# Optimization experiments

Hardware: AMD Instinct MI355X
Metric: run time of the kernel (lower is better)

The kernel has to match this reference:

```python
import jax, jax.numpy as jnp
import numpy as np

B, H, L, DK, DV = 2, 16, 2048, 64, 64


def setup_inputs() -> dict:
    key = jax.random.key(0)
    kq, kk, kv, km = jax.random.split(key, 4)
    return {
        "Q": jax.random.normal(kq, (B, H, L, DK), dtype=jnp.float32),
        "K": jax.random.normal(kk, (B, H, L, DK), dtype=jnp.float32),
        "V": jax.random.normal(kv, (B, H, L, DV), dtype=jnp.float32),
        "attn_mask": jax.random.uniform(km, (L, L), dtype=jnp.float32),
        "d_k": DK,
    }


def reference(Q, K, V, attn_mask, d_k):
    # scores: [B, H, L, L]
    scale = 1.0 / np.sqrt(d_k).astype(np.float32)
    scores = jnp.einsum("bhqd,bhkd->bhqk", Q, K) * scale
    attn = jax.nn.softmax(scores, axis=-1)
    # MSE-style loss vs a 2-D target mask broadcast over (B, H)
    diff = attn - attn_mask[None, None, :, :]
    loss = jnp.sum(diff * diff)
    context = jnp.einsum("bhqk,bhkd->bhqd", attn, V)
    return (context, loss)
```

## Files before the change

kernel.cpp:

```cpp
#include <hip/hip_runtime.h>

#define NHEAD 32
#define LSEQ  2048
#define DIM   64
#define QBLK  64
#define KBLK  64
#define NTILE (LSEQ / KBLK)

typedef float  f32x4  __attribute__((ext_vector_type(4)));
typedef __bf16 bf16x8 __attribute__((ext_vector_type(8)));
typedef unsigned short u16;

__device__ __forceinline__ u16 f2bf(float f) {
    return __builtin_bit_cast(u16, (__bf16)f);
}
__device__ __forceinline__ void st4bf(u16* p, float4 v) {
    union { u16 h[4]; uint2 q; } pk;
    pk.h[0] = f2bf(v.x); pk.h[1] = f2bf(v.y);
    pk.h[2] = f2bf(v.z); pk.h[3] = f2bf(v.w);
    *(uint2*)p = pk.q;
}
__device__ __forceinline__ bf16x8 comb64(const u16* a, const u16* b) {
    union { uint2 q[2]; bf16x8 v; } u;
    u.q[0] = *(const uint2*)a;
    u.q[1] = *(const uint2*)b;
    return u.v;
}

#define QSCALE 0.18033688011112042f
#define RESCALE_THR 8.0f

__launch_bounds__(256, 4)
__global__ void attn_fused_kernel(const float* __restrict__ Q,
                                  const float* __restrict__ K,
                                  const float* __restrict__ V,
                                  const float* __restrict__ Msk,
                                  float* __restrict__ out,
                                  float* __restrict__ loss)
{
    __shared__ __align__(16) u16 lds_k[64][72];
    __shared__ __align__(16) u16 lds_v[64][68];

    const int t  = threadIdx.x;
    const int wg   = ((int)blockIdx.x & 7) * 128 + ((int)blockIdx.x >> 3);
    const int head = wg >> 5;
    const int qb   = wg & 31;
    const int qbase = qb * QBLK;
    const int w  = t >> 6;
    const int l  = t & 63;
    const int lr = l & 15;
    const int lq = l >> 4;

    const size_t hoff = (size_t)head * LSEQ * DIM;
    const int qg = qbase + 16 * w + lr;

    bf16x8 qf[2];
#pragma unroll
    for (int s = 0; s < 2; ++s) {
        const float* src = Q + hoff + (size_t)qg * DIM + 32 * s + 8 * lq;
        float4 a = *(const float4*)(src);
        float4 b = *(const float4*)(src + 4);
        union { u16 h[8]; bf16x8 v; } u;
        u.h[0] = f2bf(a.x * QSCALE); u.h[1] = f2bf(a.y * QSCALE);
        u.h[2] = f2bf(a.z * QSCALE); u.h[3] = f2bf(a.w * QSCALE);
        u.h[4] = f2bf(b.x * QSCALE); u.h[5] = f2bf(b.y * QSCALE);
        u.h[6] = f2bf(b.z * QSCALE); u.h[7] = f2bf(b.w * QSCALE);
        qf[s] = u.v;
    }

    f32x4 acc[4];
#pragma unroll
    for (int dt = 0; dt < 4; ++dt) acc[dt] = (f32x4){0.f, 0.f, 0.f, 0.f};
    float mrun = -1e30f, lrun = 0.f, la2 = 0.f, lam = 0.f;

    for (int kb = 0; kb < NTILE; ++kb) {
        const int kbase = kb * KBLK;
        __syncthreads();

        f32x4 mreg[4];
        {
            const float* mp_ = Msk + (size_t)qg * LSEQ + kbase + 4 * lq;
#pragma unroll
            for (int m = 0; m < 4; ++m)
                mreg[m] = *(const f32x4*)(mp_ + 16 * m);
        }

        {
            const float* Kg = K + hoff + (size_t)kbase * DIM;
            const float* Vg = V + hoff + (size_t)kbase * DIM;
#pragma unroll
            for (int i = 0; i < 4; ++i) {
                const int id = t + 256 * i;
                const int r = id >> 4, c = (id & 15) * 4;
                float4 kv = *(const float4*)(Kg + r * DIM + c);
                float4 vv = *(const float4*)(Vg + r * DIM + c);
                st4bf(&lds_k[r][c], kv);
                lds_v[c + 0][r] = f2bf(vv.x);
                lds_v[c + 1][r] = f2bf(vv.y);
                lds_v[c + 2][r] = f2bf(vv.z);
                lds_v[c + 3][r] = f2bf(vv.w);
            }
        }
        __syncthreads();

        f32x4 S[4];
#pragma unroll
        for (int m = 0; m < 4; ++m) {
            bf16x8 kf0 = *(const bf16x8*)&lds_k[16 * m + lr][8 * lq];
            bf16x8 kf1 = *(const bf16x8*)&lds_k[16 * m + lr][32 + 8 * lq];
            f32x4 z = (f32x4){0.f, 0.f, 0.f, 0.f};
            z = __builtin_amdgcn_mfma_f32_16x16x32_bf16(kf0, qf[0], z, 0, 0, 0);
            z = __builtin_amdgcn_mfma_f32_16x16x32_bf16(kf1, qf[1], z, 0, 0, 0);
            S[m] = z;
        }

        float tm = fmaxf(fmaxf(fmaxf(S[0][0], S[0][1]), fmaxf(S[0][2], S[0][3])),
                         fmaxf(fmaxf(S[1][0], S[1][1]), fmaxf(S[1][2], S[1][3])));
        tm = fmaxf(tm, fmaxf(fmaxf(fmaxf(S[2][0], S[2][1]), fmaxf(S[2][2], S[2][3])),
                             fmaxf(fmaxf(S[3][0], S[3][1]), fmaxf(S[3][2], S[3][3]))));
        tm = fmaxf(tm, __shfl_xor(tm, 16));
        tm = fmaxf(tm, __shfl_xor(tm, 32));
        if (!__all(tm - mrun <= RESCALE_THR)) {
            const float mn = fmaxf(mrun, tm);
            const float al = __builtin_amdgcn_exp2f(mrun - mn);
            mrun = mn;
            lrun *= al; la2 *= al * al; lam *= al;
#pragma unroll
            for (int dt = 0; dt < 4; ++dt) acc[dt] *= al;
        }

        float psum = 0.f, pp2 = 0.f, ppm = 0.f;
        u16 pb[16];
#pragma unroll
        for (int m = 0; m < 4; ++m) {
#pragma unroll
            for (int r = 0; r < 4; ++r) {
                float p = __builtin_amdgcn_exp2f(S[m][r] - mrun);
                psum += p;
                pp2  += p * p;
                ppm  += p * mreg[m][r];
                pb[4 * m + r] = f2bf(p);
            }
        }
        lrun += psum; la2 += pp2; lam += ppm;

        bf16x8 pf[2];
#pragma unroll
        for (int mp = 0; mp < 2; ++mp) {
            union { u16 h[8]; bf16x8 v; } u;
#pragma unroll
            for (int j = 0; j < 4; ++j) { u.h[j] = pb[8 * mp + j]; u.h[4 + j] = pb[8 * mp + 4 + j]; }
            pf[mp] = u.v;
        }
#pragma unroll
        for (int dt = 0; dt < 4; ++dt) {
#pragma unroll
            for (int mp = 0; mp < 2; ++mp) {
                bf16x8 vf = comb64(&lds_v[16 * dt + lr][32 * mp + 4 * lq],
                                   &lds_v[16 * dt + lr][32 * mp + 16 + 4 * lq]);
                acc[dt] = __builtin_amdgcn_mfma_f32_16x16x32_bf16(vf, pf[mp], acc[dt], 0, 0, 0);
            }
        }
    }

#pragma unroll
    for (int off = 16; off <= 32; off <<= 1) {
        lrun += __shfl_xor(lrun, off);
        la2  += __shfl_xor(la2,  off);
        lam  += __shfl_xor(lam,  off);
    }

    const float inv = 1.0f / lrun;

#pragma unroll
    for (int dt = 0; dt < 4; ++dt) {
        float4 o;
        o.x = acc[dt][0] * inv; o.y = acc[dt][1] * inv;
        o.z = acc[dt][2] * inv; o.w = acc[dt][3] * inv;
        *(float4*)(out + hoff + (size_t)qg * DIM + 16 * dt + 4 * lq) = o;
    }

    float part = la2 * inv * inv - 2.0f * lam * inv;
    part = (l < 16) ? part : 0.f;
#pragma unroll
    for (int off = 1; off <= 8; off <<= 1) part += __shfl_xor(part, off);
    if (l == 0) atomicAdd(loss, part);
}

__global__ void masksq_kernel(const float* __restrict__ Msk, float* __restrict__ loss)
{
    __shared__ float red[4];
    float s = 0.f;
    const size_t n4 = (size_t)LSEQ * LSEQ / 4;
    for (size_t i = (size_t)blockIdx.x * blockDim.x + threadIdx.x; i < n4;
         i += (size_t)gridDim.x * blockDim.x) {
        float4 v = ((const float4*)Msk)[i];
        s += v.x * v.x + v.y * v.y + v.z * v.z + v.w * v.w;
    }
#pragma unroll
    for (int off = 1; off <= 32; off <<= 1) s += __shfl_xor(s, off);
    if ((threadIdx.x & 63) == 0) red[threadIdx.x >> 6] = s;
    __syncthreads();
    if (threadIdx.x == 0) {
        float tot = red[0] + red[1] + red[2] + red[3];
        atomicAdd(loss, 32.0f * tot);
    }
}

extern "C" void kernel_launch(void* const* d_in, const int* in_sizes, int n_in,
                              void* d_out, int out_size, void* d_ws, size_t ws_size,
                              hipStream_t stream)
{
    const float* Q   = (const float*)d_in[0];
    const float* K   = (const float*)d_in[1];
    const float* V   = (const float*)d_in[2];
    const float* Msk = (const float*)d_in[3];
    float* out  = (float*)d_out;
    float* loss = out + (size_t)NHEAD * LSEQ * DIM;

    hipMemsetAsync(loss, 0, sizeof(float), stream);
    masksq_kernel<<<256, 256, 0, stream>>>(Msk, loss);
    attn_fused_kernel<<<NHEAD * (LSEQ / QBLK), 256, 0, stream>>>(Q, K, V, Msk, out, loss);
}
```

Baseline: 147.6 us.

## Prepack K/V to swizzled bf16 tiles and double-buffer via direct global-to-LDS loads

Adds a prepack kernel that converts K and V to bf16 once per call, using an XOR-swizzled tile layout with V already transposed, and writes them to the workspace. The attention kernel then streams each tile into double-buffered LDS with global_load_lds, prefetching the next tile while computing the current one. It also raises wave priority around the MFMA blocks. This removes the 32x redundant fp32 K/V conversion per query block and halves K/V read traffic, at the cost of an extra launch, workspace use, and twice the LDS per block. Without enough workspace it falls back to the old kernel.

Measured after the change: 147.1 us. No clear change (-0.4%).

```diff
diff --git a/kernel.cpp b/kernel.cpp
--- a/kernel.cpp
+++ b/kernel.cpp
@@ -27,19 +27,77 @@
     return u.v;
 }
 
+__device__ __forceinline__ void gl_lds16(const u16* g, u16* l) {
+    __builtin_amdgcn_global_load_lds(
+        (const __attribute__((address_space(1))) void*)g,
+        (__attribute__((address_space(3))) void*)l, 16, 0, 0);
+}
+
+#define TILE_SYNC() asm volatile("s_waitcnt vmcnt(0)\n\ts_barrier" ::: "memory")
+
 #define QSCALE 0.18033688011112042f
 #define RESCALE_THR 8.0f
 
+__global__ void prepack_kernel(const float* __restrict__ K,
+                               const float* __restrict__ V,
+                               u16* __restrict__ wsK, u16* __restrict__ wsV)
+{
+    __shared__ float sv[64][65];
+    const int b = blockIdx.x;
+    const int head = b >> 5, kb = b & 31;
+    const int t = threadIdx.x;
+    const size_t hoff = (size_t)head * LSEQ * DIM;
+    const float* Kg = K + hoff + (size_t)(kb * KBLK) * DIM;
+    const float* Vg = V + hoff + (size_t)(kb * KBLK) * DIM;
+    u16* outK = wsK + (size_t)b * 4096;
+    u16* outV = wsV + (size_t)b * 4096;
+
+#pragma unroll
+    for (int i = 0; i < 16; ++i) {
+        const int e = t + 256 * i;
+        sv[e >> 6][e & 63] = Vg[e];
+    }
+#pragma unroll
+    for (int i = 0; i < 2; ++i) {
+        const int c = t + 256 * i;
+        const int r = c >> 3, q = c & 7;
+        const int d0 = 8 * (q ^ (r & 7));
+        float4 a  = *(const float4*)(Kg + r * DIM + d0);
+        float4 bb = *(const float4*)(Kg + r * DIM + d0 + 4);
+        union { u16 h[8]; uint4 u; } pk;
+        pk.h[0]=f2bf(a.x);  pk.h[1]=f2bf(a.y);  pk.h[2]=f2bf(a.z);  pk.h[3]=f2bf(a.w);
+        pk.h[4]=f2bf(bb.x); pk.h[5]=f2bf(bb.y); pk.h[6]=f2bf(bb.z); pk.h[7]=f2bf(bb.w);
+        *(uint4*)(outK + c * 8) = pk.u;
+    }
+    __syncthreads();
+#pragma unroll
+    for (int i = 0; i < 2; ++i) {
+        const int c = t + 256 * i;
+        const int d = c >> 3, q = c & 7;
+        const int cl = q ^ (d & 7);
+        const int mp = cl >> 2, lq = cl & 3;
+        union { u16 h[8]; uint4 u; } pk;
+#pragma unroll
+        for (int s = 0; s < 2; ++s) {
+            const int k0 = 4 * (8 * mp + 4 * s + lq);
+#pragma unroll
+            for (int j = 0; j < 4; ++j)
+                pk.h[4 * s + j] = f2bf(sv[k0 + j][d]);
+        }
+        *(uint4*)(outV + c * 8) = pk.u;
+    }
+}
+
 __launch_bounds__(256, 4)
 __global__ void attn_fused_kernel(const float* __restrict__ Q,
-                                  const float* __restrict__ K,
-                                  const float* __restrict__ V,
+                                  const u16* __restrict__ wsK,
+                                  const u16* __restrict__ wsV,
                                   const float* __restrict__ Msk,
                                   float* __restrict__ out,
                                   float* __restrict__ loss)
 {
-    __shared__ __align__(16) u16 lds_k[64][72];
-    __shared__ __align__(16) u16 lds_v[64][68];
+    __shared__ __align__(16) u16 lds_k[2][4096];
+    __shared__ __align__(16) u16 lds_v[2][4096];
 
     const int t  = threadIdx.x;
     const int wg   = ((int)blockIdx.x & 7) * 128 + ((int)blockIdx.x >> 3);
@@ -50,6 +108,7 @@
     const int l  = t & 63;
     const int lr = l & 15;
     const int lq = l >> 4;
+    const int x7 = lr & 7;
 
     const size_t hoff = (size_t)head * LSEQ * DIM;
     const int qg = qbase + 16 * w + lr;
@@ -73,10 +132,170 @@
     for (int dt = 0; dt < 4; ++dt) acc[dt] = (f32x4){0.f, 0.f, 0.f, 0.f};
     float mrun = -1e30f, lrun = 0.f, la2 = 0.f, lam = 0.f;
 
+    const u16* srcK = wsK + (size_t)(head * NTILE) * 4096 + t * 8;
+    const u16* srcV = wsV + (size_t)(head * NTILE) * 4096 + t * 8;
+
+    auto stage = [&](int buf, int kb) {
+        const u16* gk = srcK + (size_t)kb * 4096;
+        const u16* gv = srcV + (size_t)kb * 4096;
+        gl_lds16(gk,        &lds_k[buf][t * 8]);
+        gl_lds16(gk + 2048, &lds_k[buf][t * 8 + 2048]);
+        gl_lds16(gv,        &lds_v[buf][t * 8]);
+        gl_lds16(gv + 2048, &lds_v[buf][t * 8 + 2048]);
+    };
+
+    stage(0, 0);
+    int cur = 0;
+
+    for (int kb = 0; kb < NTILE; ++kb) {
+        TILE_SYNC();
+
+        f32x4 mreg[4];
+        {
+            const float* mp_ = Msk + (size_t)qg * LSEQ + kb * KBLK + 4 * lq;
+#pragma unroll
+            for (int m = 0; m < 4; ++m)
+                mreg[m] = *(const f32x4*)(mp_ + 16 * m);
+        }
+
+        if (kb + 1 < NTILE) stage(cur ^ 1, kb + 1);
+
+        f32x4 S[4];
+        __builtin_amdgcn_s_setprio(1);
+#pragma unroll
+        for (int m = 0; m < 4; ++m) {
+            const u16* kro = &lds_k[cur][(16 * m + lr) * 64];
+            bf16x8 kf0 = *(const bf16x8*)(kro + ((lq ^ x7) << 3));
+            bf16x8 kf1 = *(const bf16x8*)(kro + (((lq + 4) ^ x7) << 3));
+            f32x4 z = (f32x4){0.f, 0.f, 0.f, 0.f};
+            z = __builtin_amdgcn_mfma_f32_16x16x32_bf16(kf0, qf[0], z, 0, 0, 0);
+            z = __builtin_amdgcn_mfma_f32_16x16x32_bf16(kf1, qf[1], z, 0, 0, 0);
+            S[m] = z;
+        }
+        __builtin_amdgcn_s_setprio(0);
+
+        float tm = fmaxf(fmaxf(fmaxf(S[0][0], S[0][1]), fmaxf(S[0][2], S[0][3])),
+                         fmaxf(fmaxf(S[1][0], S[1][1]), fmaxf(S[1][2], S[1][3])));
+        tm = fmaxf(tm, fmaxf(fmaxf(fmaxf(S[2][0], S[2][1]), fmaxf(S[2][2], S[2][3])),
+                             fmaxf(fmaxf(S[3][0], S[3][1]), fmaxf(S[3][2], S[3][3]))));
+        tm = fmaxf(tm, __shfl_xor(tm, 16));
+        tm = fmaxf(tm, __shfl_xor(tm, 32));
+        if (!__all(tm - mrun <= RESCALE_THR)) {
+            const float mn = fmaxf(mrun, tm);
+            const float al = __builtin_amdgcn_exp2f(mrun - mn);
+            mrun = mn;
+            lrun *= al; la2 *= al * al; lam *= al;
+#pragma unroll
+            for (int dt = 0; dt < 4; ++dt) acc[dt] *= al;
+        }
+
+        float psum = 0.f, pp2 = 0.f, ppm = 0.f;
+        u16 pb[16];
+#pragma unroll
+        for (int m = 0; m < 4; ++m) {
+#pragma unroll
+            for (int r = 0; r < 4; ++r) {
+                float p = __builtin_amdgcn_exp2f(S[m][r] - mrun);
+                psum += p;
+                pp2  += p * p;
+                ppm  += p * mreg[m][r];
+                pb[4 * m + r] = f2bf(p);
+            }
+        }
+        lrun += psum; la2 += pp2; lam += ppm;
+
+        bf16x8 pf[2];
+#pragma unroll
+        for (int mp = 0; mp < 2; ++mp) {
+            union { u16 h[8]; bf16x8 v; } u;
+#pragma unroll
+            for (int j = 0; j < 4; ++j) { u.h[j] = pb[8 * mp + j]; u.h[4 + j] = pb[8 * mp + 4 + j]; }
+            pf[mp] = u.v;
+        }
+        __builtin_amdgcn_s_setprio(1);
+#pragma unroll
+        for (int dt = 0; dt < 4; ++dt) {
+            const u16* vro = &lds_v[cur][(16 * dt + lr) * 64];
+#pragma unroll
+            for (int mp = 0; mp < 2; ++mp) {
+                bf16x8 vf = *(const bf16x8*)(vro + (((4 * mp + lq) ^ x7) << 3));
+                acc[dt] = __builtin_amdgcn_mfma_f32_16x16x32_bf16(vf, pf[mp], acc[dt], 0, 0, 0);
+            }
+        }
+        __builtin_amdgcn_s_setprio(0);
+        cur ^= 1;
+    }
+
+#pragma unroll
+    for (int off = 16; off <= 32; off <<= 1) {
+        lrun += __shfl_xor(lrun, off);
+        la2  += __shfl_xor(la2,  off);
+        lam  += __shfl_xor(lam,  off);
+    }
+
+    const float inv = 1.0f / lrun;
+
+#pragma unroll
+    for (int dt = 0; dt < 4; ++dt) {
+        float4 o;
+        o.x = acc[dt][0] * inv; o.y = acc[dt][1] * inv;
+        o.z = acc[dt][2] * inv; o.w = acc[dt][3] * inv;
+        *(float4*)(out + hoff + (size_t)qg * DIM + 16 * dt + 4 * lq) = o;
+    }
+
+    float part = la2 * inv * inv - 2.0f * lam * inv;
+    part = (l < 16) ? part : 0.f;
+#pragma unroll
+    for (int off = 1; off <= 8; off <<= 1) part += __shfl_xor(part, off);
+    if (l == 0) atomicAdd(loss, part);
+}
+
+__launch_bounds__(256, 4)
+__global__ void attn_fallback_kernel(const float* __restrict__ Q,
+                                     const float* __restrict__ K,
+                                     const float* __restrict__ V,
+                                     const float* __restrict__ Msk,
+                                     float* __restrict__ out,
+                                     float* __restrict__ loss)
+{
+    __shared__ __align__(16) u16 lds_k[64][72];
+    __shared__ __align__(16) u16 lds_v[64][68];
+
+    const int t  = threadIdx.x;
+    const int wg   = ((int)blockIdx.x & 7) * 128 + ((int)blockIdx.x >> 3);
+    const int head = wg >> 5;
+    const int qb   = wg & 31;
+    const int qbase = qb * QBLK;
+    const int w  = t >> 6;
+    const int l  = t & 63;
+    const int lr = l & 15;
+    const int lq = l >> 4;
+
+    const size_t hoff = (size_t)head * LSEQ * DIM;
+    const int qg = qbase + 16 * w + lr;
+
+    bf16x8 qf[2];
+#pragma unroll
+    for (int s = 0; s < 2; ++s) {
+        const float* src = Q + hoff + (size_t)qg * DIM + 32 * s + 8 * lq;
+        float4 a = *(const float4*)(src);
+        float4 b = *(const float4*)(src + 4);
+        union { u16 h[8]; bf16x8 v; } u;
+        u.h[0] = f2bf(a.x * QSCALE); u.h[1] = f2bf(a.y * QSCALE);
+        u.h[2] = f2bf(a.z * QSCALE); u.h[3] = f2bf(a.w * QSCALE);
+        u.h[4] = f2bf(b.x * QSCALE); u.h[5] = f2bf(b.y * QSCALE);
+        u.h[6] = f2bf(b.z * QSCALE); u.h[7] = f2bf(b.w * QSCALE);
+        qf[s] = u.v;
+    }
+
+    f32x4 acc[4];
+#pragma unroll
+    for (int dt = 0; dt < 4; ++dt) acc[dt] = (f32x4){0.f, 0.f, 0.f, 0.f};
+    float mrun = -1e30f, lrun = 0.f, la2 = 0.f, lam = 0.f;
+
     for (int kb = 0; kb < NTILE; ++kb) {
         const int kbase = kb * KBLK;
         __syncthreads();
-
         f32x4 mreg[4];
         {
             const float* mp_ = Msk + (size_t)qg * LSEQ + kbase + 4 * lq;
@@ -84,7 +303,6 @@
             for (int m = 0; m < 4; ++m)
                 mreg[m] = *(const f32x4*)(mp_ + 16 * m);
         }
-
         {
             const float* Kg = K + hoff + (size_t)kbase * DIM;
             const float* Vg = V + hoff + (size_t)kbase * DIM;
@@ -169,9 +387,7 @@
         la2  += __shfl_xor(la2,  off);
         lam  += __shfl_xor(lam,  off);
     }
-
     const float inv = 1.0f / lrun;
-
 #pragma unroll
     for (int dt = 0; dt < 4; ++dt) {
         float4 o;
@@ -179,7 +395,6 @@
         o.z = acc[dt][2] * inv; o.w = acc[dt][3] * inv;
         *(float4*)(out + hoff + (size_t)qg * DIM + 16 * dt + 4 * lq) = o;
     }
-
     float part = la2 * inv * inv - 2.0f * lam * inv;
     part = (l < 16) ? part : 0.f;
 #pragma unroll
@@ -220,5 +435,14 @@
 
     hipMemsetAsync(loss, 0, sizeof(float), stream);
     masksq_kernel<<<256, 256, 0, stream>>>(Msk, loss);
-    attn_fused_kernel<<<NHEAD * (LSEQ / QBLK), 256, 0, stream>>>(Q, K, V, Msk, out, loss);
-}
+
+    const size_t need = (size_t)2 * NHEAD * NTILE * 4096 * sizeof(u16);
+    if (d_ws && ws_size >= need) {
+        u16* wsK = (u16*)d_ws;
+        u16* wsV = wsK + (size_t)NHEAD * NTILE * 4096;
+        prepack_kernel<<<NHEAD * NTILE, 256, 0, stream>>>(K, V, wsK, wsV);
+        attn_fused_kernel<<<NHEAD * (LSEQ / QBLK), 256, 0, stream>>>(Q, wsK, wsV, Msk, out, loss);
+    } else {
+        attn_fallback_kernel<<<NHEAD * (LSEQ / QBLK), 256, 0, stream>>>(Q, K, V, Msk, out, loss);
+    }
+}
```
